# Kernel tuning notes

Hardware: AMD Instinct MI355X
Metric: run time of the kernel (lower is better)

## Reference

```python
import jax, jax.numpy as jnp
import numpy as np

B, S, H = 2, 2048, 2048
NH, NKV = 16, 4
HD = H // NH          # 128
N_REP = NH // NKV     # 4


def _rotate_half(x):
    x1, x2 = x[..., : x.shape[-1] // 2], x[..., x.shape[-1] // 2 :]
    return jnp.concatenate((-x2, x1), axis=-1)


def setup_inputs() -> dict:
    key = jax.random.key(0)
    ks = jax.random.split(key, 5)
    hidden_states = jax.random.normal(ks[0], (B, S, H), dtype=jnp.float32)
    # true rotary tables [max_seq_len, head_dim]
    inv_freq = 1.0 / (10000.0 ** (np.arange(0, HD, 2, dtype=np.float32) / HD))
    t = np.arange(S, dtype=np.float32)
    freqs = np.outer(t, inv_freq)                    # [S, HD/2]
    emb = np.concatenate([freqs, freqs], axis=-1)    # [S, HD]
    cos = jnp.asarray(np.cos(emb))
    sin = jnp.asarray(np.sin(emb))
    Wq = jax.random.normal(ks[1], (H, NH * HD), dtype=jnp.float32) * 0.02
    Wk = jax.random.normal(ks[2], (H, NKV * HD), dtype=jnp.float32) * 0.02
    Wv = jax.random.normal(ks[3], (H, NKV * HD), dtype=jnp.float32) * 0.02
    Wo = jax.random.normal(ks[4], (NH * HD, H), dtype=jnp.float32) * 0.02
    attention_mask = jnp.ones((B, S), dtype=jnp.float32)  # 1 = keep
    return {"hidden_states": hidden_states, "cos": cos, "sin": sin,
            "Wq": Wq, "Wk": Wk, "Wv": Wv, "Wo": Wo,
            "attention_mask": attention_mask}


def reference(hidden_states, cos, sin, Wq, Wk, Wv, Wo, attention_mask):
    # Decoder self-attention: is_causal=True, use_rope=True, no cache, eval (dropout off).
    x = hidden_states
    b, s, _ = x.shape
    q = jnp.einsum('bsh,hd->bsd', x, Wq).reshape(b, s, NH, HD).transpose(0, 2, 1, 3)   # [b,nh,s,hd]
    k = jnp.einsum('bsh,hd->bsd', x, Wk).reshape(b, s, NKV, HD)
    v = jnp.einsum('bsh,hd->bsd', x, Wv).reshape(b, s, NKV, HD)
    # GQA repeat_kv: each kv head repeated n_rep times contiguously
    k = jnp.repeat(k, N_REP, axis=2).transpose(0, 2, 1, 3)   # [b,nh,s,hd]
    v = jnp.repeat(v, N_REP, axis=2).transpose(0, 2, 1, 3)
    # RoPE
    c = cos[:s][None, None, :, :]
    sn = sin[:s][None, None, :, :]
    q = q * c + _rotate_half(q) * sn
    k = k * c + _rotate_half(k) * sn
    # attention scores
    scores = jnp.einsum('bhqd,bhkd->bhqk', q, k) / jnp.sqrt(jnp.float32(HD))
    neg_inf = jnp.finfo(scores.dtype).min
    causal = jnp.triu(jnp.full((s, s), neg_inf, dtype=scores.dtype), k=1)
    scores = scores + causal[None, None, :, :]
    pad = (1.0 - attention_mask[:, None, None, :].astype(scores.dtype)) * neg_inf
    scores = scores + pad
    attn = jax.nn.softmax(scores.astype(jnp.float32), axis=-1).astype(q.dtype)
    out = jnp.einsum('bhqk,bhkd->bhqd', attn, v)             # [b,nh,s,hd]
    out = out.transpose(0, 2, 1, 3).reshape(b, s, NH * HD)
    return jnp.einsum('bsd,dh->bsh', out, Wo)
```

## Files before the change

kernel.cpp:

```cpp
#include <hip/hip_runtime.h>
#include <hip/hip_bf16.h>


typedef __bf16 bf16;
typedef __bf16 bf16x8 __attribute__((ext_vector_type(8)));
typedef __bf16 bf16x4 __attribute__((ext_vector_type(4)));
typedef float  f32x4  __attribute__((ext_vector_type(4)));

#define MFMA_BF16(a, b, c) __builtin_amdgcn_mfma_f32_16x16x32_bf16((a), (b), (c), 0, 0, 0)

__device__ __forceinline__ void glds16(const bf16* g, char* l) {
  __builtin_amdgcn_global_load_lds((__attribute__((address_space(1))) const void*)g,
                                   (__attribute__((address_space(3))) void*)l, 16, 0, 0);
}

__global__ __launch_bounds__(256) void k_cvt_bf16(const float* __restrict__ in,
                                                  bf16* __restrict__ out, int n4) {
  int i = blockIdx.x * 256 + threadIdx.x;
  if (i < n4) {
    float4 v = ((const float4*)in)[i];
    bf16x4 o;
    o[0] = (bf16)v.x; o[1] = (bf16)v.y; o[2] = (bf16)v.z; o[3] = (bf16)v.w;
    ((bf16x4*)out)[i] = o;
  }
}

__global__ __launch_bounds__(256) void k_transpose_w(const float* __restrict__ W,
                                                     bf16* __restrict__ Wt, int Kd, int N) {
  __shared__ float tile[32][33];
  int tx = threadIdx.x, ty = threadIdx.y;
  int kb = blockIdx.x * 32, nb = blockIdx.y * 32;
#pragma unroll
  for (int i = 0; i < 4; ++i)
    tile[ty + i * 8][tx] = W[(size_t)(kb + ty + i * 8) * N + nb + tx];
  __syncthreads();
#pragma unroll
  for (int i = 0; i < 4; ++i)
    Wt[(size_t)(nb + ty + i * 8) * Kd + kb + tx] = (bf16)tile[tx][ty + i * 8];
}

__global__ __launch_bounds__(256) void k_transpose_v(const bf16* __restrict__ V,
                                                     bf16* __restrict__ Vt) {
  __shared__ bf16 tile[32][33];
  int tx = threadIdx.x, ty = threadIdx.y;
  int b = blockIdx.z;
  int sb = blockIdx.x * 32, cb = blockIdx.y * 32;
#pragma unroll
  for (int i = 0; i < 4; ++i)
    tile[ty + i * 8][tx] = V[(size_t)(b * 2048 + sb + ty + i * 8) * 512 + cb + tx];
  __syncthreads();
#pragma unroll
  for (int i = 0; i < 4; ++i)
    Vt[(size_t)(b * 512 + cb + ty + i * 8) * 2048 + sb + tx] = tile[tx][ty + i * 8];
}

__global__ __launch_bounds__(256) void k_rope(bf16* __restrict__ T,
                                              const float* __restrict__ cosb,
                                              const float* __restrict__ sinb,
                                              int ncols, float scl) {
  int i = blockIdx.x * 256 + threadIdx.x;
  int npr = ncols >> 1;
  int row = i / npr;
  int p = i - row * npr;
  int h = p >> 6, d = p & 63;
  int c0 = h * 128 + d;
  size_t base = (size_t)row * ncols;
  int s = row & 2047;
  float q0 = (float)T[base + c0];
  float q1 = (float)T[base + c0 + 64];
  float vc0 = cosb[s * 128 + d],      vc1 = cosb[s * 128 + d + 64];
  float vs0 = sinb[s * 128 + d],      vs1 = sinb[s * 128 + d + 64];
  T[base + c0]      = (bf16)((q0 * vc0 - q1 * vs0) * scl);
  T[base + c0 + 64] = (bf16)((q1 * vc1 + q0 * vs1) * scl);
}

template <typename OUT>
__device__ void gemm_block(const bf16* __restrict__ A, const bf16* __restrict__ Bt,
                           OUT* __restrict__ C, int K, int ldc,
                           int rbase, int cbase, char* sm) {
  const int tid = threadIdx.x;
  const int lane = tid & 63, wid = tid >> 6;
  const int l15 = lane & 15, lg = lane >> 4;
  char* Asm = sm;
  char* Bsm = sm + 32768;

  f32x4 acc[2][8];
#pragma unroll
  for (int i = 0; i < 2; ++i)
#pragma unroll
    for (int j = 0; j < 8; ++j)
#pragma unroll
      for (int r = 0; r < 4; ++r) acc[i][j][r] = 0.0f;

  const int ob = wid * 4096 + lane * 16;
  auto stage = [&](int buf, int kb) {
#pragma unroll
    for (int c = 0; c < 4; ++c) {
      int o = ob + c * 1024;
      int r = o >> 7;
      int cc = ((o >> 4) & 7) ^ (r & 7);
      int dst = wid * 4096 + c * 1024 + buf * 16384;
      glds16(A + (size_t)(rbase + r) * K + kb + cc * 8, Asm + dst);
      glds16(Bt + (size_t)(cbase + r) * K + kb + cc * 8, Bsm + dst);
    }
  };

  stage(0, 0);
  __syncthreads();
  const int nk = K >> 6;
  for (int t = 0; t < nk; ++t) {
    if (t + 1 < nk) stage((t + 1) & 1, (t + 1) << 6);
    const char* At  = Asm + (t & 1) * 16384;
    const char* Bti = Bsm + (t & 1) * 16384;
#pragma unroll
    for (int ks = 0; ks < 2; ++ks) {
      bf16x8 a[2], b[8];
#pragma unroll
      for (int rf = 0; rf < 2; ++rf) {
        int r = wid * 32 + rf * 16 + l15;
        int slot = (ks * 4 + lg) ^ (r & 7);
        a[rf] = *(const bf16x8*)(At + r * 128 + slot * 16);
      }
#pragma unroll
      for (int nf = 0; nf < 8; ++nf) {
        int n = nf * 16 + l15;
        int slot = (ks * 4 + lg) ^ (n & 7);
        b[nf] = *(const bf16x8*)(Bti + n * 128 + slot * 16);
      }
#pragma unroll
      for (int rf = 0; rf < 2; ++rf)
#pragma unroll
        for (int nf = 0; nf < 8; ++nf)
          acc[rf][nf] = MFMA_BF16(a[rf], b[nf], acc[rf][nf]);
    }
    __syncthreads();
  }

#pragma unroll
  for (int rf = 0; rf < 2; ++rf)
#pragma unroll
    for (int nf = 0; nf < 8; ++nf)
#pragma unroll
      for (int r = 0; r < 4; ++r) {
        int row = rbase + wid * 32 + rf * 16 + lg * 4 + r;
        int col = cbase + nf * 16 + l15;
        C[(size_t)row * ldc + col] = (OUT)acc[rf][nf][r];
      }
}

__global__ __launch_bounds__(256, 2) void k_gemm_qkv(const bf16* __restrict__ X,
                                                     const bf16* __restrict__ Wtq,
                                                     const bf16* __restrict__ Wtk,
                                                     const bf16* __restrict__ Wtv,
                                                     bf16* __restrict__ Q,
                                                     bf16* __restrict__ Ko,
                                                     bf16* __restrict__ Vo) {
  __shared__ alignas(16) char sm[65536];
  int nb = blockIdx.y;
  int rbase = blockIdx.x * 128;
  const bf16* Bt; bf16* C; int ldc, cbase;
  if (nb < 16)      { Bt = Wtq; C = Q;  ldc = 2048; cbase = nb * 128; }
  else if (nb < 20) { Bt = Wtk; C = Ko; ldc = 512;  cbase = (nb - 16) * 128; }
  else              { Bt = Wtv; C = Vo; ldc = 512;  cbase = (nb - 20) * 128; }
  gemm_block<bf16>(X, Bt, C, 2048, ldc, rbase, cbase, sm);
}

__global__ __launch_bounds__(256, 2) void k_gemm_o(const bf16* __restrict__ AO,
                                                   const bf16* __restrict__ Wto,
                                                   float* __restrict__ Out) {
  __shared__ alignas(16) char sm[65536];
  gemm_block<float>(AO, Wto, Out, 2048, 2048, blockIdx.x * 128, blockIdx.y * 128, sm);
}

__global__ __launch_bounds__(256, 4) void k_fattn(const bf16* __restrict__ Qg,
                                                  const bf16* __restrict__ Kg,
                                                  const bf16* __restrict__ Vtg,
                                                  bf16* __restrict__ AO) {
  __shared__ alignas(16) char sm[37888];
  const int lane = threadIdx.x & 63, wid = threadIdx.x >> 6;
  const int l15 = lane & 15, lg = lane >> 4;
  const int wg = blockIdx.x;
  const int grp = wg & 7;
  const int b = grp >> 2, kv = grp & 3;
  const int inner = wg >> 3;
  const int h = kv * 4 + (inner & 3);
  const int strip = 31 - (inner >> 2);
  const int q0 = strip * 64 + wid * 16;
  const int nt = 2 * (strip + 1);
  char* Pw = sm + 32768 + wid * 1280;

  bf16x8 qf[4];
#pragma unroll
  for (int kf = 0; kf < 4; ++kf)
    qf[kf] = *(const bf16x8*)(Qg + (size_t)(b * 2048 + q0 + l15) * 2048 + h * 128 + kf * 32 + lg * 8);

  f32x4 o[8];
#pragma unroll
  for (int j = 0; j < 8; ++j)
#pragma unroll
    for (int r = 0; r < 4; ++r) o[j][r] = 0.0f;
  float mrun = -3e38f, lrun = 0.0f;

  auto stageKV = [&](int buf, int kb) {
#pragma unroll
    for (int j = 0; j < 2; ++j) {
      int c = wid * 128 + j * 64 + lane;
      int kr = c >> 4, kslot = c & 15;
      int kcc = kslot ^ (kr & 15);
      glds16(Kg + (size_t)(b * 2048 + kb + kr) * 512 + kv * 128 + kcc * 8,
             sm + buf * 8192 + wid * 2048 + j * 1024);
      int vr = c >> 2, vslot = c & 3;
      int vcc = vslot ^ ((vr >> 1) & 3);
      glds16(Vtg + (size_t)((b * 4 + kv) * 128 + vr) * 2048 + kb + vcc * 8,
             sm + 16384 + buf * 8192 + wid * 2048 + j * 1024);
    }
  };

  stageKV(0, 0);
  __syncthreads();

  for (int t = 0; t < nt; ++t) {
    const int kb = t << 5;
    if (t + 1 < nt) stageKV((t + 1) & 1, kb + 32);
    const char* Kt = sm + (t & 1) * 8192;
    const char* Vt = sm + 16384 + (t & 1) * 8192;

    f32x4 sa[2];
#pragma unroll
    for (int j = 0; j < 2; ++j)
#pragma unroll
      for (int r = 0; r < 4; ++r) sa[j][r] = 0.0f;
#pragma unroll
    for (int kf = 0; kf < 4; ++kf) {
#pragma unroll
      for (int nf = 0; nf < 2; ++nf) {
        int slot = (kf * 4 + lg) ^ l15;
        bf16x8 bk = *(const bf16x8*)(Kt + (nf * 16 + l15) * 256 + slot * 16);
        sa[nf] = MFMA_BF16(bk, qf[kf], sa[nf]);
      }
    }

    if (kb + 31 > q0) {
      const int qi = q0 + l15;
#pragma unroll
      for (int nf = 0; nf < 2; ++nf)
#pragma unroll
        for (int r = 0; r < 4; ++r)
          if (kb + nf * 16 + lg * 4 + r > qi) sa[nf][r] = -3e38f;
    }

    float mx = sa[0][0];
#pragma unroll
    for (int nf = 0; nf < 2; ++nf)
#pragma unroll
      for (int r = 0; r < 4; ++r) mx = fmaxf(mx, sa[nf][r]);
    mx = fmaxf(mx, __shfl_xor(mx, 16));
    mx = fmaxf(mx, __shfl_xor(mx, 32));
    if (!__all(mx - mrun <= 8.0f)) {
      float mnew = fmaxf(mrun, mx);
      float fac = __builtin_amdgcn_exp2f(mrun - mnew);
      lrun *= fac;
      f32x4 fv;
#pragma unroll
      for (int r = 0; r < 4; ++r) fv[r] = __shfl(fac, lg * 4 + r);
#pragma unroll
      for (int j = 0; j < 8; ++j) o[j] *= fv;
      mrun = mnew;
    }
    float rs = 0.0f;
#pragma unroll
    for (int nf = 0; nf < 2; ++nf) {
      bf16x4 pk;
#pragma unroll
      for (int r = 0; r < 4; ++r) {
        float p = __builtin_amdgcn_exp2f(sa[nf][r] - mrun);
        rs += p;
        pk[r] = (bf16)p;
      }
      *(bf16x4*)(Pw + l15 * 80 + nf * 32 + lg * 8) = pk;
    }
    rs += __shfl_xor(rs, 16);
    rs += __shfl_xor(rs, 32);
    lrun += rs;

    bf16x8 pa = *(const bf16x8*)(Pw + l15 * 80 + lg * 16);
#pragma unroll
    for (int nf2 = 0; nf2 < 8; ++nf2) {
      int d = nf2 * 16 + l15;
      int slot = lg ^ ((d >> 1) & 3);
      bf16x8 vb = *(const bf16x8*)(Vt + d * 64 + slot * 16);
      o[nf2] = MFMA_BF16(pa, vb, o[nf2]);
    }
    __syncthreads();
  }

  f32x4 linv;
#pragma unroll
  for (int r = 0; r < 4; ++r) linv[r] = 1.0f / __shfl(lrun, lg * 4 + r);
#pragma unroll
  for (int j = 0; j < 8; ++j)
#pragma unroll
    for (int r = 0; r < 4; ++r) {
      size_t row = (size_t)(b * 2048 + q0 + lg * 4 + r);
      AO[row * 2048 + h * 128 + j * 16 + l15] = (bf16)(o[j][r] * linv[r]);
    }
}

extern "C" void kernel_launch(void* const* d_in, const int* in_sizes, int n_in,
                              void* d_out, int out_size, void* d_ws, size_t ws_size,
                              hipStream_t stream) {
  const float* hs   = (const float*)d_in[0];
  const float* cosb = (const float*)d_in[1];
  const float* sinb = (const float*)d_in[2];
  const float* Wq   = (const float*)d_in[3];
  const float* Wk   = (const float*)d_in[4];
  const float* Wv   = (const float*)d_in[5];
  const float* Wo   = (const float*)d_in[6];
  float* Out = (float*)d_out;

  char* ws = (char*)d_ws;
  size_t off = 0;
  auto alloc = [&](size_t bytes) { char* p = ws + off; off += bytes; return p; };
  bf16* Xbf = (bf16*)alloc((size_t)4096 * 2048 * 2);
  bf16* Wtq = (bf16*)alloc((size_t)2048 * 2048 * 2);
  bf16* Wtk = (bf16*)alloc((size_t)512 * 2048 * 2);
  bf16* Wtv = (bf16*)alloc((size_t)512 * 2048 * 2);
  bf16* Wto = (bf16*)alloc((size_t)2048 * 2048 * 2);
  bf16* Qb  = (bf16*)alloc((size_t)4096 * 2048 * 2);
  bf16* Kb  = (bf16*)alloc((size_t)4096 * 512 * 2);
  bf16* Vb  = (bf16*)alloc((size_t)4096 * 512 * 2);
  bf16* Vtb = (bf16*)alloc((size_t)4096 * 512 * 2);
  bf16* AO  = (bf16*)alloc((size_t)4096 * 2048 * 2);

  const float SCLQ = 0.08838834764831845f * 1.4426950408889634f;

  dim3 tb(32, 8);
  k_cvt_bf16<<<8192, 256, 0, stream>>>(hs, Xbf, 2097152);
  k_transpose_w<<<dim3(64, 64), tb, 0, stream>>>(Wq, Wtq, 2048, 2048);
  k_transpose_w<<<dim3(64, 16), tb, 0, stream>>>(Wk, Wtk, 2048, 512);
  k_transpose_w<<<dim3(64, 16), tb, 0, stream>>>(Wv, Wtv, 2048, 512);
  k_transpose_w<<<dim3(64, 64), tb, 0, stream>>>(Wo, Wto, 2048, 2048);
  k_gemm_qkv<<<dim3(32, 24), 256, 0, stream>>>(Xbf, Wtq, Wtk, Wtv, Qb, Kb, Vb);
  k_rope<<<16384, 256, 0, stream>>>(Qb, cosb, sinb, 2048, SCLQ);
  k_rope<<<4096, 256, 0, stream>>>(Kb, cosb, sinb, 512, 1.0f);
  k_transpose_v<<<dim3(64, 16, 2), tb, 0, stream>>>(Vb, Vtb);
  k_fattn<<<1024, 256, 0, stream>>>(Qb, Kb, Vtb, AO);
  k_gemm_o<<<dim3(32, 16), 256, 0, stream>>>(AO, Wto, Out);
}
```

Measured before the change: 209.2 us.

## Fuse RoPE into QKV GEMM epilogue, merge weight transposes, interleave attention strips

RoPE and the Q scaling now run inside the QKV GEMM epilogue on the fp32 accumulators. This removes two separate read-modify-write passes over Q and K and two kernel launches. The four weight-transpose launches are merged into one 3D-grid launch, with early exit for blocks past the narrower K/V matrices. The flash-attention kernel now interleaves long and short causal strips in block order to balance load, and it precomputes its K/V staging addresses and advances them by pointer increments. The epilogue adds per-element cos/sin global loads, and RoPE is now applied before bf16 rounding, which slightly changes numerics.

```diff
diff --git a/kernel.cpp b/kernel.cpp
--- a/kernel.cpp
+++ b/kernel.cpp
@@ -25,18 +25,32 @@
   }
 }
 
-__global__ __launch_bounds__(256) void k_transpose_w(const float* __restrict__ W,
-                                                     bf16* __restrict__ Wt, int Kd, int N) {
+__global__ __launch_bounds__(256) void k_transpose_w4(const float* __restrict__ Wq,
+                                                      const float* __restrict__ Wk,
+                                                      const float* __restrict__ Wv,
+                                                      const float* __restrict__ Wo,
+                                                      bf16* __restrict__ Wtq,
+                                                      bf16* __restrict__ Wtk,
+                                                      bf16* __restrict__ Wtv,
+                                                      bf16* __restrict__ Wto) {
+  int z = blockIdx.z;
+  const float* W; bf16* Wt; int N;
+  if (z == 0)      { W = Wq; Wt = Wtq; N = 2048; }
+  else if (z == 1) { W = Wo; Wt = Wto; N = 2048; }
+  else if (z == 2) { W = Wk; Wt = Wtk; N = 512; }
+  else             { W = Wv; Wt = Wtv; N = 512; }
+  int nb = blockIdx.y * 32;
+  if (nb >= N) return;
   __shared__ float tile[32][33];
   int tx = threadIdx.x, ty = threadIdx.y;
-  int kb = blockIdx.x * 32, nb = blockIdx.y * 32;
+  int kb = blockIdx.x * 32;
 #pragma unroll
   for (int i = 0; i < 4; ++i)
     tile[ty + i * 8][tx] = W[(size_t)(kb + ty + i * 8) * N + nb + tx];
   __syncthreads();
 #pragma unroll
   for (int i = 0; i < 4; ++i)
-    Wt[(size_t)(nb + ty + i * 8) * Kd + kb + tx] = (bf16)tile[tx][ty + i * 8];
+    Wt[(size_t)(nb + ty + i * 8) * 2048 + kb + tx] = (bf16)tile[tx][ty + i * 8];
 }
 
 __global__ __launch_bounds__(256) void k_transpose_v(const bf16* __restrict__ V,
@@ -54,30 +68,12 @@
     Vt[(size_t)(b * 512 + cb + ty + i * 8) * 2048 + sb + tx] = tile[tx][ty + i * 8];
 }
 
-__global__ __launch_bounds__(256) void k_rope(bf16* __restrict__ T,
-                                              const float* __restrict__ cosb,
-                                              const float* __restrict__ sinb,
-                                              int ncols, float scl) {
-  int i = blockIdx.x * 256 + threadIdx.x;
-  int npr = ncols >> 1;
-  int row = i / npr;
-  int p = i - row * npr;
-  int h = p >> 6, d = p & 63;
-  int c0 = h * 128 + d;
-  size_t base = (size_t)row * ncols;
-  int s = row & 2047;
-  float q0 = (float)T[base + c0];
-  float q1 = (float)T[base + c0 + 64];
-  float vc0 = cosb[s * 128 + d],      vc1 = cosb[s * 128 + d + 64];
-  float vs0 = sinb[s * 128 + d],      vs1 = sinb[s * 128 + d + 64];
-  T[base + c0]      = (bf16)((q0 * vc0 - q1 * vs0) * scl);
-  T[base + c0 + 64] = (bf16)((q1 * vc1 + q0 * vs1) * scl);
-}
-
 template <typename OUT>
 __device__ void gemm_block(const bf16* __restrict__ A, const bf16* __restrict__ Bt,
                            OUT* __restrict__ C, int K, int ldc,
-                           int rbase, int cbase, char* sm) {
+                           int rbase, int cbase, char* sm,
+                           float rope_scl, const float* __restrict__ cosb,
+                           const float* __restrict__ sinb) {
   const int tid = threadIdx.x;
   const int lane = tid & 63, wid = tid >> 6;
   const int l15 = lane & 15, lg = lane >> 4;
@@ -136,6 +132,24 @@
     __syncthreads();
   }
 
+  if (rope_scl != 0.0f) {
+#pragma unroll
+    for (int rf = 0; rf < 2; ++rf)
+#pragma unroll
+      for (int r = 0; r < 4; ++r) {
+        int s = (rbase + wid * 32 + rf * 16 + lg * 4 + r) & 2047;
+#pragma unroll
+        for (int nf = 0; nf < 4; ++nf) {
+          int d = nf * 16 + l15;
+          float v0 = acc[rf][nf][r], v1 = acc[rf][nf + 4][r];
+          float c0 = cosb[s * 128 + d],      c1 = cosb[s * 128 + d + 64];
+          float s0 = sinb[s * 128 + d],      s1 = sinb[s * 128 + d + 64];
+          acc[rf][nf][r]     = (v0 * c0 - v1 * s0) * rope_scl;
+          acc[rf][nf + 4][r] = (v1 * c1 + v0 * s1) * rope_scl;
+        }
+      }
+  }
+
 #pragma unroll
   for (int rf = 0; rf < 2; ++rf)
 #pragma unroll
@@ -154,22 +168,26 @@
                                                      const bf16* __restrict__ Wtv,
                                                      bf16* __restrict__ Q,
                                                      bf16* __restrict__ Ko,
-                                                     bf16* __restrict__ Vo) {
+                                                     bf16* __restrict__ Vo,
+                                                     const float* __restrict__ cosb,
+                                                     const float* __restrict__ sinb,
+                                                     float sclq) {
   __shared__ alignas(16) char sm[65536];
   int nb = blockIdx.y;
   int rbase = blockIdx.x * 128;
-  const bf16* Bt; bf16* C; int ldc, cbase;
-  if (nb < 16)      { Bt = Wtq; C = Q;  ldc = 2048; cbase = nb * 128; }
-  else if (nb < 20) { Bt = Wtk; C = Ko; ldc = 512;  cbase = (nb - 16) * 128; }
-  else              { Bt = Wtv; C = Vo; ldc = 512;  cbase = (nb - 20) * 128; }
-  gemm_block<bf16>(X, Bt, C, 2048, ldc, rbase, cbase, sm);
+  const bf16* Bt; bf16* C; int ldc, cbase; float rs;
+  if (nb < 16)      { Bt = Wtq; C = Q;  ldc = 2048; cbase = nb * 128;        rs = sclq; }
+  else if (nb < 20) { Bt = Wtk; C = Ko; ldc = 512;  cbase = (nb - 16) * 128; rs = 1.0f; }
+  else              { Bt = Wtv; C = Vo; ldc = 512;  cbase = (nb - 20) * 128; rs = 0.0f; }
+  gemm_block<bf16>(X, Bt, C, 2048, ldc, rbase, cbase, sm, rs, cosb, sinb);
 }
 
 __global__ __launch_bounds__(256, 2) void k_gemm_o(const bf16* __restrict__ AO,
                                                    const bf16* __restrict__ Wto,
                                                    float* __restrict__ Out) {
   __shared__ alignas(16) char sm[65536];
-  gemm_block<float>(AO, Wto, Out, 2048, 2048, blockIdx.x * 128, blockIdx.y * 128, sm);
+  gemm_block<float>(AO, Wto, Out, 2048, 2048, blockIdx.x * 128, blockIdx.y * 128, sm,
+                    0.0f, nullptr, nullptr);
 }
 
 __global__ __launch_bounds__(256, 4) void k_fattn(const bf16* __restrict__ Qg,
@@ -184,7 +202,8 @@
   const int b = grp >> 2, kv = grp & 3;
   const int inner = wg >> 3;
   const int h = kv * 4 + (inner & 3);
-  const int strip = 31 - (inner >> 2);
+  const int si = inner >> 2;
+  const int strip = (si & 1) ? (si >> 1) : (31 - (si >> 1));
   const int q0 = strip * 64 + wid * 16;
   const int nt = 2 * (strip + 1);
   char* Pw = sm + 32768 + wid * 1280;
@@ -201,27 +220,37 @@
     for (int r = 0; r < 4; ++r) o[j][r] = 0.0f;
   float mrun = -3e38f, lrun = 0.0f;
 
-  auto stageKV = [&](int buf, int kb) {
+  const bf16* ksrc[2];
+  const bf16* vsrc[2];
+  int kdst[2], vdst[2];
+#pragma unroll
+  for (int j = 0; j < 2; ++j) {
+    int c = wid * 128 + j * 64 + lane;
+    int kr = c >> 4, kslot = c & 15;
+    int kcc = kslot ^ (kr & 15);
+    ksrc[j] = Kg + (size_t)(b * 2048 + kr) * 512 + kv * 128 + kcc * 8;
+    kdst[j] = wid * 2048 + j * 1024;
+    int vr = c >> 2, vslot = c & 3;
+    int vcc = vslot ^ ((vr >> 1) & 3);
+    vsrc[j] = Vtg + (size_t)((b * 4 + kv) * 128 + vr) * 2048 + vcc * 8;
+    vdst[j] = 16384 + wid * 2048 + j * 1024;
+  }
+  auto stageKV = [&](int buf) {
 #pragma unroll
     for (int j = 0; j < 2; ++j) {
-      int c = wid * 128 + j * 64 + lane;
-      int kr = c >> 4, kslot = c & 15;
-      int kcc = kslot ^ (kr & 15);
-      glds16(Kg + (size_t)(b * 2048 + kb + kr) * 512 + kv * 128 + kcc * 8,
-             sm + buf * 8192 + wid * 2048 + j * 1024);
-      int vr = c >> 2, vslot = c & 3;
-      int vcc = vslot ^ ((vr >> 1) & 3);
-      glds16(Vtg + (size_t)((b * 4 + kv) * 128 + vr) * 2048 + kb + vcc * 8,
-             sm + 16384 + buf * 8192 + wid * 2048 + j * 1024);
+      glds16(ksrc[j], sm + buf * 8192 + kdst[j]);
+      glds16(vsrc[j], sm + buf * 8192 + vdst[j]);
+      ksrc[j] += 32 * 512;
+      vsrc[j] += 32;
     }
   };
 
-  stageKV(0, 0);
+  stageKV(0);
   __syncthreads();
 
   for (int t = 0; t < nt; ++t) {
     const int kb = t << 5;
-    if (t + 1 < nt) stageKV((t + 1) & 1, kb + 32);
+    if (t + 1 < nt) stageKV((t + 1) & 1);
     const char* Kt = sm + (t & 1) * 8192;
     const char* Vt = sm + 16384 + (t & 1) * 8192;
 
@@ -336,13 +365,9 @@
 
   dim3 tb(32, 8);
   k_cvt_bf16<<<8192, 256, 0, stream>>>(hs, Xbf, 2097152);
-  k_transpose_w<<<dim3(64, 64), tb, 0, stream>>>(Wq, Wtq, 2048, 2048);
-  k_transpose_w<<<dim3(64, 16), tb, 0, stream>>>(Wk, Wtk, 2048, 512);
-  k_transpose_w<<<dim3(64, 16), tb, 0, stream>>>(Wv, Wtv, 2048, 512);
-  k_transpose_w<<<dim3(64, 64), tb, 0, stream>>>(Wo, Wto, 2048, 2048);
-  k_gemm_qkv<<<dim3(32, 24), 256, 0, stream>>>(Xbf, Wtq, Wtk, Wtv, Qb, Kb, Vb);
-  k_rope<<<16384, 256, 0, stream>>>(Qb, cosb, sinb, 2048, SCLQ);
-  k_rope<<<4096, 256, 0, stream>>>(Kb, cosb, sinb, 512, 1.0f);
+  k_transpose_w4<<<dim3(64, 64, 4), tb, 0, stream>>>(Wq, Wk, Wv, Wo, Wtq, Wtk, Wtv, Wto);
+  k_gemm_qkv<<<dim3(32, 24), 256, 0, stream>>>(Xbf, Wtq, Wtk, Wtv, Qb, Kb, Vb,
+                                               cosb, sinb, SCLQ);
   k_transpose_v<<<dim3(64, 16, 2), tb, 0, stream>>>(Vb, Vtb);
   k_fattn<<<1024, 256, 0, stream>>>(Qb, Kb, Vtb, AO);
   k_gemm_o<<<dim3(32, 16), 256, 0, stream>>>(AO, Wto, Out);
```

After: 202.6 us. 1.03x faster.
